# Kernel tuning notes

Hardware: AMD Instinct MI355X
Metric: run time of the kernel (lower is better)

The kernel has to match this reference:

```python
import jax, jax.numpy as jnp
import numpy as np

D_MODEL = 256
N_HEADS = 8
D_HEAD = D_MODEL // N_HEADS
SCALE = D_HEAD ** -0.5
LN_EPS = 1e-5


def _layernorm(x, gamma, beta):
    mu = jnp.mean(x, axis=-1, keepdims=True)
    var = jnp.mean(jnp.square(x - mu), axis=-1, keepdims=True)
    return (x - mu) * jax.lax.rsqrt(var + LN_EPS) * gamma + beta


def setup_inputs() -> dict:
    key = jax.random.key(0)
    ks = jax.random.split(key, 8)
    B, N_q, N_kv = 2, 1024, 8192
    q = jax.random.normal(ks[0], (B, N_q, D_MODEL), dtype=jnp.float32)
    kv = jax.random.normal(ks[1], (B, N_kv, D_MODEL), dtype=jnp.float32)
    attn_bias = jax.random.normal(ks[2], (B, N_HEADS, N_q, N_kv), dtype=jnp.float32)
    s = D_MODEL ** -0.5
    Wq = jax.random.normal(ks[3], (D_MODEL, D_MODEL), dtype=jnp.float32) * s
    Wk = jax.random.normal(ks[4], (D_MODEL, D_MODEL), dtype=jnp.float32) * s
    Wv = jax.random.normal(ks[5], (D_MODEL, D_MODEL), dtype=jnp.float32) * s
    Wo = jax.random.normal(ks[6], (D_MODEL, D_MODEL), dtype=jnp.float32) * s
    gamma_q = jnp.ones((D_MODEL,), jnp.float32)
    beta_q = jnp.zeros((D_MODEL,), jnp.float32)
    gamma_kv = jnp.ones((D_MODEL,), jnp.float32)
    beta_kv = jnp.zeros((D_MODEL,), jnp.float32)
    return dict(q=q, kv=kv, attn_bias=attn_bias, Wq=Wq, Wk=Wk, Wv=Wv, Wo=Wo,
                gamma_q=gamma_q, beta_q=beta_q, gamma_kv=gamma_kv, beta_kv=beta_kv)


def reference(q, kv, attn_bias, Wq, Wk, Wv, Wo, gamma_q, beta_q, gamma_kv, beta_kv):
    B, N_q, D = q.shape
    N_kv = kv.shape[1]
    q_n = _layernorm(q, gamma_q, beta_q)
    kv_n = _layernorm(kv, gamma_kv, beta_kv)
    # nn.Linear(x) = x @ W.T ; reshape to (B, H, N, dh)
    Q = (q_n @ Wq.T).reshape(B, N_q, N_HEADS, D_HEAD).transpose(0, 2, 1, 3)
    K = (kv_n @ Wk.T).reshape(B, N_kv, N_HEADS, D_HEAD).transpose(0, 2, 1, 3)
    V = (kv_n @ Wv.T).reshape(B, N_kv, N_HEADS, D_HEAD).transpose(0, 2, 1, 3)
    scores = jnp.einsum('bhqd,bhkd->bhqk', Q, K) * SCALE + attn_bias
    attn = jax.nn.softmax(scores, axis=-1)
    out = jnp.einsum('bhqk,bhkd->bhqd', attn, V)
    out = out.transpose(0, 2, 1, 3).reshape(B, N_q, D)
    return q + out @ Wo.T
```

## Files before the change

### kernel.cpp

```cpp
#include <hip/hip_runtime.h>
#include <hip/hip_bf16.h>
#include <stdint.h>

#define H 8
#define NQ 1024
#define NKV 8192
#define DM 256
#define DH 32
#define KVBLK 128
#define KSPLIT 8
#define KSLICE (NKV / KSPLIT)
#define NITER (KSLICE / KVBLK)
#define SCALE 0.17677669529663687f

typedef __attribute__((ext_vector_type(8))) __bf16 bf16x8;
typedef __attribute__((ext_vector_type(4))) float f32x4;

__device__ inline unsigned short f2bf(float f) {
  unsigned int u = __builtin_bit_cast(unsigned int, f);
  u = (u + 0x7FFFu + ((u >> 16) & 1u)) >> 16;
  return (unsigned short)u;
}

__global__ void prep_kernel(const float* __restrict__ q, const float* __restrict__ kv,
                            const float* __restrict__ gq, const float* __restrict__ bq,
                            const float* __restrict__ gkv, const float* __restrict__ bkv,
                            const float* __restrict__ Wq, const float* __restrict__ Wk,
                            const float* __restrict__ Wv, const float* __restrict__ Wo,
                            unsigned short* __restrict__ qn, unsigned short* __restrict__ kvn,
                            unsigned short* __restrict__ Wqb, unsigned short* __restrict__ Wkb,
                            unsigned short* __restrict__ Wvb, unsigned short* __restrict__ Wob) {
  int bx = blockIdx.x;
  if (bx < 256) {
    int widx = bx >> 6, blk = bx & 63;
    const float* src; unsigned short* dst;
    if (widx == 0)      { src = Wq; dst = Wqb; }
    else if (widx == 1) { src = Wk; dst = Wkb; }
    else if (widx == 2) { src = Wv; dst = Wvb; }
    else                { src = Wo; dst = Wob; }
    int i = (blk * 256 + threadIdx.x) * 4;
    float4 v = *(const float4*)(src + i);
    unsigned int lo = (unsigned int)f2bf(v.x) | ((unsigned int)f2bf(v.y) << 16);
    unsigned int hi = (unsigned int)f2bf(v.z) | ((unsigned int)f2bf(v.w) << 16);
    *(uint2*)(dst + i) = make_uint2(lo, hi);
    return;
  }
  int row = (bx - 256) * 64 + (threadIdx.x >> 2);
  int l4 = threadIdx.x & 3;
  const float* src; const float* ga; const float* be; unsigned short* dst;
  if (row < 2048) {
    src = q + (long)row * DM; ga = gq; be = bq; dst = qn + (long)row * DM;
  } else {
    int r2 = row - 2048;
    src = kv + (long)r2 * DM; ga = gkv; be = bkv; dst = kvn + (long)r2 * DM;
  }
  int c0 = l4 * 64;
  float s = 0.f, ss = 0.f;
  float4 xv[16];
#pragma unroll
  for (int i = 0; i < 16; i++) {
    float4 v = *(const float4*)(src + c0 + i * 4);
    xv[i] = v;
    s += v.x + v.y + v.z + v.w;
    ss += v.x * v.x + v.y * v.y + v.z * v.z + v.w * v.w;
  }
  s += __shfl_xor(s, 1, 4);  s += __shfl_xor(s, 2, 4);
  ss += __shfl_xor(ss, 1, 4); ss += __shfl_xor(ss, 2, 4);
  float mean = s * (1.0f / 256.0f);
  float var = ss * (1.0f / 256.0f) - mean * mean;
  float rs = 1.0f / sqrtf(var + 1e-5f);
#pragma unroll
  for (int i = 0; i < 8; i++) {
    float4 a = xv[2 * i], b = xv[2 * i + 1];
    float4 g0 = *(const float4*)(ga + c0 + i * 8);
    float4 g1 = *(const float4*)(ga + c0 + i * 8 + 4);
    float4 b0 = *(const float4*)(be + c0 + i * 8);
    float4 b1 = *(const float4*)(be + c0 + i * 8 + 4);
    unsigned short t[8];
    t[0] = f2bf((a.x - mean) * rs * g0.x + b0.x);
    t[1] = f2bf((a.y - mean) * rs * g0.y + b0.y);
    t[2] = f2bf((a.z - mean) * rs * g0.z + b0.z);
    t[3] = f2bf((a.w - mean) * rs * g0.w + b0.w);
    t[4] = f2bf((b.x - mean) * rs * g1.x + b1.x);
    t[5] = f2bf((b.y - mean) * rs * g1.y + b1.y);
    t[6] = f2bf((b.z - mean) * rs * g1.z + b1.z);
    t[7] = f2bf((b.w - mean) * rs * g1.w + b1.w);
    unsigned int u0 = (unsigned int)t[0] | ((unsigned int)t[1] << 16);
    unsigned int u1 = (unsigned int)t[2] | ((unsigned int)t[3] << 16);
    unsigned int u2 = (unsigned int)t[4] | ((unsigned int)t[5] << 16);
    unsigned int u3 = (unsigned int)t[6] | ((unsigned int)t[7] << 16);
    *(uint4*)(dst + c0 + i * 8) = make_uint4(u0, u1, u2, u3);
  }
}

__global__ void proj_all_kernel(const unsigned short* __restrict__ qn, const unsigned short* __restrict__ kvn,
                                const unsigned short* __restrict__ Wqb, const unsigned short* __restrict__ Wkb,
                                const unsigned short* __restrict__ Wvb,
                                unsigned short* __restrict__ Qw, unsigned short* __restrict__ Kw,
                                unsigned short* __restrict__ Vtw) {
  int bx = blockIdx.x;
  const unsigned short* X; const unsigned short* Wb; unsigned short* out;
  int Nper, mode, mb;
  if (bx < 32)       { X = qn;  Wb = Wqb; out = Qw;  Nper = NQ;  mode = 0; mb = bx; }
  else if (bx < 288) { X = kvn; Wb = Wkb; out = Kw;  Nper = NKV; mode = 0; mb = bx - 32; }
  else               { X = kvn; Wb = Wvb; out = Vtw; Nper = NKV; mode = 1; mb = bx - 288; }

  int w = threadIdx.x >> 6, lane = threadIdx.x & 63;
  int c = lane & 15, g = lane >> 4;
  int mbase = mb * 64 + w * 16;
  f32x4 acc[16];
#pragma unroll
  for (int i = 0; i < 16; i++) acc[i] = (f32x4){0.f, 0.f, 0.f, 0.f};
  const unsigned short* arow = X + (long)(mbase + c) * DM + g * 8;
#pragma unroll
  for (int ks = 0; ks < 8; ks++) {
    bf16x8 af = *(const bf16x8*)(arow + ks * 32);
#pragma unroll
    for (int nt = 0; nt < 16; nt++) {
      bf16x8 bf = *(const bf16x8*)(Wb + (long)(nt * 16 + c) * DM + ks * 32 + g * 8);
      acc[nt] = __builtin_amdgcn_mfma_f32_16x16x32_bf16(af, bf, acc[nt], 0, 0, 0);
    }
  }
#pragma unroll
  for (int nt = 0; nt < 16; nt++) {
#pragma unroll
    for (int r = 0; r < 4; r++) {
      int m = mbase + 4 * g + r;
      int n = nt * 16 + c;
      int b = (m >= Nper) ? 1 : 0;
      int i = m - b * Nper;
      int h = n >> 5, dd = n & 31;
      long idx;
      if (mode == 0) idx = ((long)(b * H + h) * Nper + i) * DH + dd;
      else           idx = ((long)(b * H + h) * DH + dd) * (long)Nper + i;
      out[idx] = f2bf(acc[nt][r]);
    }
  }
}

__global__ __launch_bounds__(256, 4) void attn_kernel(
    const unsigned short* __restrict__ Qw, const unsigned short* __restrict__ Kw,
    const unsigned short* __restrict__ Vtw, const float* __restrict__ bias,
    float* __restrict__ Opart, float* __restrict__ Mpart, float* __restrict__ Lpart) {
  __shared__ __align__(16) unsigned short Klds[KVBLK * 40];
  __shared__ __align__(16) unsigned short Vlds[DH * 136];
  __shared__ __align__(16) unsigned short Plds[4][16 * 136];

  int bx = blockIdx.x;
  int s = bx & 7, qt = (bx >> 3) & 15, bh = bx >> 7;
  int tid = threadIdx.x;
  int w = tid >> 6, lane = tid & 63, c = lane & 15, g = lane >> 4;

  const f32x4 fzero = {0.f, 0.f, 0.f, 0.f};

  bf16x8 qfrag = *(const bf16x8*)(Qw + ((long)(bh * NQ + qt * 64 + w * 16 + c)) * DH + g * 8);

  const float* brow = bias + ((long)bh * NQ + qt * 64 + w * 16 + c) * (long)NKV
                      + s * KSLICE + 4 * g;

  const unsigned short* Kbase = Kw + ((long)bh * NKV + s * KSLICE) * DH;
  const unsigned short* Vbase = Vtw + ((long)bh * DH) * NKV + s * KSLICE;

  float m_run = -1e30f;
  float l_run = 0.f;
  f32x4 oacc[2] = {fzero, fzero};

#pragma unroll 1
  for (int it = 0; it < NITER; it++) {
    int k0 = it * KVBLK;

    f32x4 bfrag[8];
#pragma unroll
    for (int t = 0; t < 8; t++)
      bfrag[t] = *(const f32x4*)(brow + k0 + t * 16);

    {
      const unsigned short* src = Kbase + (long)k0 * DH;
#pragma unroll
      for (int rp = 0; rp < 2; rp++) {
        int row = (tid >> 2) + rp * 64;
        int q4 = tid & 3;
        *(uint4*)(&Klds[row * 40 + q4 * 8]) = *(const uint4*)(src + row * DH + q4 * 8);
      }
#pragma unroll
      for (int rp = 0; rp < 2; rp++) {
        int u = tid + rp * 256;
        int d = u >> 4, q16 = u & 15;
        *(uint4*)(&Vlds[d * 136 + q16 * 8]) = *(const uint4*)(Vbase + (long)d * NKV + k0 + q16 * 8);
      }
    }
    __syncthreads();

    f32x4 sacc[8];
#pragma unroll
    for (int t = 0; t < 8; t++) {
      bf16x8 kf = *(const bf16x8*)(&Klds[(t * 16 + c) * 40 + g * 8]);
      sacc[t] = __builtin_amdgcn_mfma_f32_16x16x32_bf16(kf, qfrag, fzero, 0, 0, 0);
    }
#pragma unroll
    for (int t = 0; t < 8; t++) {
#pragma unroll
      for (int r = 0; r < 4; r++)
        sacc[t][r] = fmaf(sacc[t][r], SCALE, bfrag[t][r]);
    }

    float v = -1e30f;
#pragma unroll
    for (int t = 0; t < 8; t++)
      v = fmaxf(v, fmaxf(fmaxf(sacc[t][0], sacc[t][1]), fmaxf(sacc[t][2], sacc[t][3])));
    v = fmaxf(v, __shfl_xor(v, 16));
    v = fmaxf(v, __shfl_xor(v, 32));
    float mnew = fmaxf(m_run, v);
    float al = __expf(m_run - mnew);
    m_run = mnew;
    float rsum = 0.f;
#pragma unroll
    for (int t = 0; t < 8; t++) {
      float p0 = __expf(sacc[t][0] - mnew);
      float p1 = __expf(sacc[t][1] - mnew);
      float p2 = __expf(sacc[t][2] - mnew);
      float p3 = __expf(sacc[t][3] - mnew);
      rsum += (p0 + p1) + (p2 + p3);
      uint2 pk;
      pk.x = (unsigned int)f2bf(p0) | ((unsigned int)f2bf(p1) << 16);
      pk.y = (unsigned int)f2bf(p2) | ((unsigned int)f2bf(p3) << 16);
      *(uint2*)(&Plds[w][c * 136 + t * 16 + 4 * g]) = pk;
    }
    rsum += __shfl_xor(rsum, 16);
    rsum += __shfl_xor(rsum, 32);
    l_run = l_run * al + rsum;

    float alq[4];
#pragma unroll
    for (int r = 0; r < 4; r++) alq[r] = __shfl(al, 4 * g + r);
#pragma unroll
    for (int r = 0; r < 4; r++) { oacc[0][r] *= alq[r]; oacc[1][r] *= alq[r]; }

#pragma unroll
    for (int ch = 0; ch < 4; ch++) {
      bf16x8 pf = *(const bf16x8*)(&Plds[w][c * 136 + ch * 32 + g * 8]);
#pragma unroll
      for (int dt = 0; dt < 2; dt++) {
        bf16x8 vf = *(const bf16x8*)(&Vlds[(dt * 16 + c) * 136 + ch * 32 + g * 8]);
        oacc[dt] = __builtin_amdgcn_mfma_f32_16x16x32_bf16(pf, vf, oacc[dt], 0, 0, 0);
      }
    }
    __syncthreads();
  }
  float* Op = Opart + (long)bx * (64 * 32);
#pragma unroll
  for (int dt = 0; dt < 2; dt++)
#pragma unroll
    for (int r = 0; r < 4; r++)
      Op[(w * 16 + 4 * g + r) * 32 + dt * 16 + c] = oacc[dt][r];
  if (g == 0) {
    Mpart[(long)bx * 64 + w * 16 + c] = m_run;
    Lpart[(long)bx * 64 + w * 16 + c] = l_run;
  }
}

__global__ void merge_outproj_kernel(const float* __restrict__ Opart, const float* __restrict__ Mpart,
                                     const float* __restrict__ Lpart, const unsigned short* __restrict__ Wob,
                                     const float* __restrict__ qin, float* __restrict__ out) {
  __shared__ __align__(16) unsigned short OmT[64][264];

  int bx = blockIdx.x;
  int b = bx >> 4, qt = bx & 15;
  int tid = threadIdx.x;

  int row = tid >> 2;
  int d0 = (tid & 3) * 8;
#pragma unroll 1
  for (int h = 0; h < 8; h++) {
    long pbase = ((long)(b * 8 + h) * 16 + qt) * 8;
    float mg = -1e30f, ms[8];
#pragma unroll
    for (int si = 0; si < 8; si++) {
      ms[si] = Mpart[(pbase + si) * 64 + row];
      mg = fmaxf(mg, ms[si]);
    }
    float Lg = 0.f;
    float o[8] = {0.f, 0.f, 0.f, 0.f, 0.f, 0.f, 0.f, 0.f};
#pragma unroll
    for (int si = 0; si < 8; si++) {
      float wsc = __expf(ms[si] - mg);
      Lg += Lpart[(pbase + si) * 64 + row] * wsc;
      const float* op = Opart + (pbase + si) * 2048 + row * 32 + d0;
#pragma unroll
      for (int j = 0; j < 8; j++) o[j] += op[j] * wsc;
    }
    float inv = 1.0f / Lg;
    unsigned int u[4];
#pragma unroll
    for (int j = 0; j < 4; j++)
      u[j] = (unsigned int)f2bf(o[2 * j] * inv) | ((unsigned int)f2bf(o[2 * j + 1] * inv) << 16);
    *(uint4*)(&OmT[row][h * 32 + d0]) = make_uint4(u[0], u[1], u[2], u[3]);
  }
  __syncthreads();

  int w = tid >> 6, lane = tid & 63;
  int c = lane & 15, g = lane >> 4;
  int mloc = w * 16;
  long mglob = (long)b * NQ + qt * 64;
  f32x4 acc[16];
#pragma unroll
  for (int i = 0; i < 16; i++) acc[i] = (f32x4){0.f, 0.f, 0.f, 0.f};
#pragma unroll
  for (int ks = 0; ks < 8; ks++) {
    bf16x8 af = *(const bf16x8*)(&OmT[mloc + c][ks * 32 + g * 8]);
#pragma unroll
    for (int nt = 0; nt < 16; nt++) {
      bf16x8 bf = *(const bf16x8*)(Wob + (long)(nt * 16 + c) * DM + ks * 32 + g * 8);
      acc[nt] = __builtin_amdgcn_mfma_f32_16x16x32_bf16(af, bf, acc[nt], 0, 0, 0);
    }
  }
#pragma unroll
  for (int nt = 0; nt < 16; nt++) {
#pragma unroll
    for (int r = 0; r < 4; r++) {
      long m = mglob + mloc + 4 * g + r;
      int n = nt * 16 + c;
      out[m * DM + n] = qin[m * DM + n] + acc[nt][r];
    }
  }
}

extern "C" void kernel_launch(void* const* d_in, const int* in_sizes, int n_in,
                              void* d_out, int out_size, void* d_ws, size_t ws_size,
                              hipStream_t stream) {
  (void)in_sizes; (void)n_in; (void)out_size; (void)ws_size;
  const float* q    = (const float*)d_in[0];
  const float* kv   = (const float*)d_in[1];
  const float* bias = (const float*)d_in[2];
  const float* Wq   = (const float*)d_in[3];
  const float* Wk   = (const float*)d_in[4];
  const float* Wv   = (const float*)d_in[5];
  const float* Wo   = (const float*)d_in[6];
  const float* gq   = (const float*)d_in[7];
  const float* bq   = (const float*)d_in[8];
  const float* gkv  = (const float*)d_in[9];
  const float* bkv  = (const float*)d_in[10];
  float* out = (float*)d_out;

  char* ws = (char*)d_ws;
  size_t off = 0;
  auto alloc = [&](size_t bytes) -> void* {
    void* p = ws + off;
    off += (bytes + 255) & ~(size_t)255;
    return p;
  };
  unsigned short* Wqb  = (unsigned short*)alloc(65536 * 2);
  unsigned short* Wkb  = (unsigned short*)alloc(65536 * 2);
  unsigned short* Wvb  = (unsigned short*)alloc(65536 * 2);
  unsigned short* Wob  = (unsigned short*)alloc(65536 * 2);
  unsigned short* qn   = (unsigned short*)alloc((size_t)2048 * 256 * 2);
  unsigned short* kvn  = (unsigned short*)alloc((size_t)16384 * 256 * 2);
  unsigned short* Qw   = (unsigned short*)alloc((size_t)2048 * 256 * 2);
  unsigned short* Kw   = (unsigned short*)alloc((size_t)16384 * 256 * 2);
  unsigned short* Vtw  = (unsigned short*)alloc((size_t)16384 * 256 * 2);
  float* Opart = (float*)alloc((size_t)2048 * 2048 * 4);
  float* Mpart = (float*)alloc((size_t)2048 * 64 * 4);
  float* Lpart = (float*)alloc((size_t)2048 * 64 * 4);

  prep_kernel<<<544, 256, 0, stream>>>(q, kv, gq, bq, gkv, bkv, Wq, Wk, Wv, Wo,
                                       qn, kvn, Wqb, Wkb, Wvb, Wob);

  proj_all_kernel<<<544, 256, 0, stream>>>(qn, kvn, Wqb, Wkb, Wvb, Qw, Kw, Vtw);

  attn_kernel<<<2048, 256, 0, stream>>>(Qw, Kw, Vtw, bias, Opart, Mpart, Lpart);

  merge_outproj_kernel<<<32, 256, 0, stream>>>(Opart, Mpart, Lpart, Wob, q, out);
}
```

Before: 269.3 us.

## Interleave KV blocks across splits and spread merge/out-proj over more blocks

The attention kernel now gives each of the 8 KV splits every 8th 128-wide block instead of a contiguous slice, so concurrent blocks touch interleaved bias/K/V regions. This likely aims to change DRAM/cache access locality. The merge+output projection kernel launches 128 blocks instead of 32, with each block handling 16 query rows and each wave computing 4 output column tiles, which adds parallelism to what was a 32-block tail kernel. The cost is more redundant loads of Wo per row and a strided KV access pattern inside each split.

After: 222.7 us. -17.3%, faster.

```diff
diff --git a/kernel.cpp b/kernel.cpp
--- a/kernel.cpp
+++ b/kernel.cpp
@@ -9,8 +9,7 @@
 #define DH 32
 #define KVBLK 128
 #define KSPLIT 8
-#define KSLICE (NKV / KSPLIT)
-#define NITER (KSLICE / KVBLK)
+#define NITER (NKV / KSPLIT / KVBLK)
 #define SCALE 0.17677669529663687f
 
 typedef __attribute__((ext_vector_type(8))) __bf16 bf16x8;
@@ -155,11 +154,10 @@
 
   bf16x8 qfrag = *(const bf16x8*)(Qw + ((long)(bh * NQ + qt * 64 + w * 16 + c)) * DH + g * 8);
 
-  const float* brow = bias + ((long)bh * NQ + qt * 64 + w * 16 + c) * (long)NKV
-                      + s * KSLICE + 4 * g;
-
-  const unsigned short* Kbase = Kw + ((long)bh * NKV + s * KSLICE) * DH;
-  const unsigned short* Vbase = Vtw + ((long)bh * DH) * NKV + s * KSLICE;
+  const float* brow = bias + ((long)bh * NQ + qt * 64 + w * 16 + c) * (long)NKV + 4 * g;
+
+  const unsigned short* Kbase = Kw + ((long)bh * NKV) * DH;
+  const unsigned short* Vbase = Vtw + ((long)bh * DH) * NKV;
 
   float m_run = -1e30f;
   float l_run = 0.f;
@@ -167,7 +165,7 @@
 
 #pragma unroll 1
   for (int it = 0; it < NITER; it++) {
-    int k0 = it * KVBLK;
+    int k0 = (it * KSPLIT + s) * KVBLK;
 
     f32x4 bfrag[8];
 #pragma unroll
@@ -262,65 +260,63 @@
 __global__ void merge_outproj_kernel(const float* __restrict__ Opart, const float* __restrict__ Mpart,
                                      const float* __restrict__ Lpart, const unsigned short* __restrict__ Wob,
                                      const float* __restrict__ qin, float* __restrict__ out) {
-  __shared__ __align__(16) unsigned short OmT[64][264];
+  __shared__ __align__(16) unsigned short OmT[16][264];
 
   int bx = blockIdx.x;
-  int b = bx >> 4, qt = bx & 15;
+  int b = bx >> 6, qt = (bx >> 2) & 15, q4 = bx & 3;
   int tid = threadIdx.x;
 
-  int row = tid >> 2;
-  int d0 = (tid & 3) * 8;
+  int row16 = tid >> 4;
+  int d0 = (tid & 15) * 2;
+  int rowA = q4 * 16 + row16;
 #pragma unroll 1
   for (int h = 0; h < 8; h++) {
     long pbase = ((long)(b * 8 + h) * 16 + qt) * 8;
     float mg = -1e30f, ms[8];
 #pragma unroll
     for (int si = 0; si < 8; si++) {
-      ms[si] = Mpart[(pbase + si) * 64 + row];
+      ms[si] = Mpart[(pbase + si) * 64 + rowA];
       mg = fmaxf(mg, ms[si]);
     }
     float Lg = 0.f;
-    float o[8] = {0.f, 0.f, 0.f, 0.f, 0.f, 0.f, 0.f, 0.f};
+    float o0 = 0.f, o1 = 0.f;
 #pragma unroll
     for (int si = 0; si < 8; si++) {
       float wsc = __expf(ms[si] - mg);
-      Lg += Lpart[(pbase + si) * 64 + row] * wsc;
-      const float* op = Opart + (pbase + si) * 2048 + row * 32 + d0;
-#pragma unroll
-      for (int j = 0; j < 8; j++) o[j] += op[j] * wsc;
+      Lg += Lpart[(pbase + si) * 64 + rowA] * wsc;
+      const float* op = Opart + (pbase + si) * 2048 + rowA * 32 + d0;
+      o0 += op[0] * wsc;
+      o1 += op[1] * wsc;
     }
     float inv = 1.0f / Lg;
-    unsigned int u[4];
-#pragma unroll
-    for (int j = 0; j < 4; j++)
-      u[j] = (unsigned int)f2bf(o[2 * j] * inv) | ((unsigned int)f2bf(o[2 * j + 1] * inv) << 16);
-    *(uint4*)(&OmT[row][h * 32 + d0]) = make_uint4(u[0], u[1], u[2], u[3]);
+    unsigned int u = (unsigned int)f2bf(o0 * inv) | ((unsigned int)f2bf(o1 * inv) << 16);
+    *(unsigned int*)(&OmT[row16][h * 32 + d0]) = u;
   }
   __syncthreads();
 
   int w = tid >> 6, lane = tid & 63;
   int c = lane & 15, g = lane >> 4;
-  int mloc = w * 16;
-  long mglob = (long)b * NQ + qt * 64;
-  f32x4 acc[16];
-#pragma unroll
-  for (int i = 0; i < 16; i++) acc[i] = (f32x4){0.f, 0.f, 0.f, 0.f};
+  long mglob = (long)b * NQ + qt * 64 + q4 * 16;
+  f32x4 acc[4];
+#pragma unroll
+  for (int i = 0; i < 4; i++) acc[i] = (f32x4){0.f, 0.f, 0.f, 0.f};
 #pragma unroll
   for (int ks = 0; ks < 8; ks++) {
-    bf16x8 af = *(const bf16x8*)(&OmT[mloc + c][ks * 32 + g * 8]);
-#pragma unroll
-    for (int nt = 0; nt < 16; nt++) {
+    bf16x8 af = *(const bf16x8*)(&OmT[c][ks * 32 + g * 8]);
+#pragma unroll
+    for (int j = 0; j < 4; j++) {
+      int nt = w * 4 + j;
       bf16x8 bf = *(const bf16x8*)(Wob + (long)(nt * 16 + c) * DM + ks * 32 + g * 8);
-      acc[nt] = __builtin_amdgcn_mfma_f32_16x16x32_bf16(af, bf, acc[nt], 0, 0, 0);
-    }
-  }
-#pragma unroll
-  for (int nt = 0; nt < 16; nt++) {
+      acc[j] = __builtin_amdgcn_mfma_f32_16x16x32_bf16(af, bf, acc[j], 0, 0, 0);
+    }
+  }
+#pragma unroll
+  for (int j = 0; j < 4; j++) {
 #pragma unroll
     for (int r = 0; r < 4; r++) {
-      long m = mglob + mloc + 4 * g + r;
-      int n = nt * 16 + c;
-      out[m * DM + n] = qin[m * DM + n] + acc[nt][r];
+      long m = mglob + 4 * g + r;
+      int n = (w * 4 + j) * 16 + c;
+      out[m * DM + n] = qin[m * DM + n] + acc[j][r];
     }
   }
 }
@@ -369,5 +365,5 @@
 
   attn_kernel<<<2048, 256, 0, stream>>>(Qw, Kw, Vtw, bias, Opart, Mpart, Lpart);
 
-  merge_outproj_kernel<<<32, 256, 0, stream>>>(Opart, Mpart, Lpart, Wob, q, out);
-}
+  merge_outproj_kernel<<<128, 256, 0, stream>>>(Opart, Mpart, Lpart, Wob, q, out);
+}
```
